# Performance work log

Hardware: AMD Instinct MI355X
Metric: run time of the kernel (lower is better)

Reference implementation:

```python
import jax, jax.numpy as jnp
import numpy as np

N_NODES = 65536
IN_DIM = 256
HIDDEN = 256
NUM_GRAPHS = 128   # B = batch.max()+1; fixed by construction in setup_inputs
MAX_LEN = 1024     # >= max per-graph length (avg 512, binomial tail << 1024)


def _uniform(key, shape, scale):
    return jax.random.uniform(key, shape, jnp.float32, -scale, scale)


def setup_inputs() -> dict:
    key = jax.random.key(0)
    ks = jax.random.split(key, 12)
    x = jax.random.normal(ks[0], (N_NODES, IN_DIM), jnp.float32)
    batch = jnp.sort(jax.random.randint(ks[1], (N_NODES,), 0, NUM_GRAPHS)).astype(jnp.int64)
    s = 1.0 / np.sqrt(HIDDEN)  # torch nn.GRU init: U(-1/sqrt(H), 1/sqrt(H))
    # gate order follows torch: (r, z, n) stacked along first axis -> 3H rows
    params = {
        'W_ih0': _uniform(ks[2], (3 * HIDDEN, IN_DIM), s),
        'W_hh0': _uniform(ks[3], (3 * HIDDEN, HIDDEN), s),
        'b_ih0': _uniform(ks[4], (3 * HIDDEN,), s),
        'b_hh0': _uniform(ks[5], (3 * HIDDEN,), s),
        'W_ih1': _uniform(ks[6], (3 * HIDDEN, HIDDEN), s),
        'W_hh1': _uniform(ks[7], (3 * HIDDEN, HIDDEN), s),
        'b_ih1': _uniform(ks[8], (3 * HIDDEN,), s),
        'b_hh1': _uniform(ks[9], (3 * HIDDEN,), s),
    }
    return {'x': x, 'batch': batch, **params}


def _gru_layer(xs, W_ih, W_hh, b_ih, b_hh):
    # xs: [B, L, D] -> [B, L, H]; torch GRU cell math, gate order (r, z, n)
    B = xs.shape[0]
    H = W_hh.shape[1]
    gx = jnp.einsum('bld,gd->blg', xs, W_ih) + b_ih  # precompute input gates, one big GEMM

    def step(h, gx_t):
        gh = h @ W_hh.T + b_hh
        xr, xz, xn = jnp.split(gx_t, 3, axis=-1)
        hr, hz, hn = jnp.split(gh, 3, axis=-1)
        r = jax.nn.sigmoid(xr + hr)
        z = jax.nn.sigmoid(xz + hz)
        n = jnp.tanh(xn + r * hn)
        h_new = (1.0 - z) * n + z * h
        return h_new, h_new

    h0 = jnp.zeros((B, H), xs.dtype)
    _, hs = jax.lax.scan(step, h0, jnp.swapaxes(gx, 0, 1))  # [L, B, H]
    return jnp.swapaxes(hs, 0, 1)


def reference(x, batch, W_ih0, W_hh0, b_ih0, b_hh0, W_ih1, W_hh1, b_ih1, b_hh1):
    # Ragged per-graph sequences -> padded [B, MAX_LEN, D]. Padding is at the
    # end of each row; GRU is causal so valid positions match the per-graph
    # loop in the original module exactly, and the masked mean ignores padding.
    N, D = x.shape
    b32 = batch.astype(jnp.int32)
    counts = jax.ops.segment_sum(jnp.ones((N,), jnp.float32), b32, num_segments=NUM_GRAPHS)
    starts = jnp.cumsum(counts) - counts              # exclusive prefix sum
    pos = jnp.arange(N, dtype=jnp.float32) - starts[b32]
    pos = pos.astype(jnp.int32)                       # position within graph

    xp = jnp.zeros((NUM_GRAPHS, MAX_LEN, D), x.dtype).at[b32, pos].set(x)
    mask = jnp.zeros((NUM_GRAPHS, MAX_LEN), x.dtype).at[b32, pos].set(1.0)

    h = _gru_layer(xp, W_ih0, W_hh0, b_ih0, b_hh0)
    h = _gru_layer(h, W_ih1, W_hh1, b_ih1, b_hh1)

    denom = jnp.maximum(counts, 1.0)[:, None]
    out = jnp.sum(h * mask[:, :, None], axis=1) / denom  # mean over valid steps
    return out  # dropout is identity at eval
```

## Files before the change

### kernel.cpp

```cpp
#include <hip/hip_runtime.h>
#include <hip/hip_bf16.h>

typedef _Float16 half2_t __attribute__((ext_vector_type(2)));
typedef _Float16 f16x8   __attribute__((ext_vector_type(8)));
typedef float    f32x4   __attribute__((ext_vector_type(4)));
typedef unsigned short u16;
typedef unsigned int   u32;

#define N_NODES 65536
#define IN_DIM  256
#define HIDDEN  256
#define G3      768
#define NGRAPH  128

__device__ __forceinline__ float sigf(float x)    { return 1.f / (1.f + __expf(-x)); }
__device__ __forceinline__ float tanhfast(float x){ return 2.f / (1.f + __expf(-2.f * x)) - 1.f; }

__global__ void k_starts(const int* __restrict__ batch, int* __restrict__ starts, int n, int ngraph) {
    int g = blockIdx.x * blockDim.x + threadIdx.x;
    if (g > ngraph) return;
    int stride = (batch[n - 1] == 0) ? 2 : 1;
    if (g == ngraph) { starts[g] = n; return; }
    int lo = 0, hi = n;
    while (lo < hi) { int mid = (lo + hi) >> 1; if (batch[(size_t)mid * stride] < g) lo = mid + 1; else hi = mid; }
    starts[g] = lo;
}

__global__ void k_cvt8(const float* __restrict__ s, u16* __restrict__ d, int n) {
    int t = blockIdx.x * 256 + threadIdx.x;
    int i = t * 8;
    if (i >= n) return;
    float4 a = ((const float4*)(s + i))[0];
    float4 b = ((const float4*)(s + i))[1];
    f16x8 o;
    o[0] = (_Float16)a.x; o[1] = (_Float16)a.y; o[2] = (_Float16)a.z; o[3] = (_Float16)a.w;
    o[4] = (_Float16)b.x; o[5] = (_Float16)b.y; o[6] = (_Float16)b.z; o[7] = (_Float16)b.w;
    *(f16x8*)(d + i) = o;
}

__global__ void k_bias(const float* __restrict__ bih, const float* __restrict__ bhh, float* __restrict__ o) {
    int i = blockIdx.x * 256 + threadIdx.x;
    if (i < G3) o[i] = bih[i] + (i < 512 ? bhh[i] : 0.f);
}

__global__ void k_swz(const float* __restrict__ W, uint4* __restrict__ out) {
    int t = blockIdx.x * 256 + threadIdx.x;
    if (t >= 24576) return;
    int l = t & 63, kt = (t >> 6) & 7, rest = t >> 9;
    int wv = rest / 6, t6 = rest % 6;
    int row = wv * 96 + t6 * 16 + (l & 15);
    int col = kt * 32 + (l >> 4) * 8;
    const float* s = W + row * 256 + col;
    f16x8 o;
#pragma unroll
    for (int q = 0; q < 8; q++) o[q] = (_Float16)s[q];
    out[t] = __builtin_bit_cast(uint4, o);
}

template <typename AT>
__global__ __launch_bounds__(256) void k_gemm(
    const AT* __restrict__ A, const u16* __restrict__ Bm,
    const float* __restrict__ bias, u16* __restrict__ C,
    int M, int N, int K)
{
    __shared__ u16 As[128 * 40];
    __shared__ u16 Bs[128 * 40];
    const int m0 = blockIdx.y * 128, n0 = blockIdx.x * 128;
    const int t = threadIdx.x;
    const int wave = t >> 6, lane = t & 63;
    const int wm = wave & 1, wn = wave >> 1;
    const int lr = lane & 15, lq = lane >> 4;
    f32x4 acc[4][4] = {};
    const int sr = t >> 1, sp = t & 1;
    const AT*  gA = A  + (size_t)(m0 + sr) * K + sp * 16;
    const u16* gB = Bm + (size_t)(n0 + sr) * K + sp * 16;
    u16* sA = As + sr * 40 + sp * 16;
    u16* sB = Bs + sr * 40 + sp * 16;
    for (int kt = 0; kt < K; kt += 32) {
        uint4 av0, av1;
        if constexpr (sizeof(AT) == 4) {
            float4 a0 = ((const float4*)gA)[0], a1 = ((const float4*)gA)[1];
            float4 a2 = ((const float4*)gA)[2], a3 = ((const float4*)gA)[3];
            f16x8 lo, hi;
            lo[0]=(_Float16)a0.x; lo[1]=(_Float16)a0.y; lo[2]=(_Float16)a0.z; lo[3]=(_Float16)a0.w;
            lo[4]=(_Float16)a1.x; lo[5]=(_Float16)a1.y; lo[6]=(_Float16)a1.z; lo[7]=(_Float16)a1.w;
            hi[0]=(_Float16)a2.x; hi[1]=(_Float16)a2.y; hi[2]=(_Float16)a2.z; hi[3]=(_Float16)a2.w;
            hi[4]=(_Float16)a3.x; hi[5]=(_Float16)a3.y; hi[6]=(_Float16)a3.z; hi[7]=(_Float16)a3.w;
            av0 = __builtin_bit_cast(uint4, lo);
            av1 = __builtin_bit_cast(uint4, hi);
        } else {
            av0 = ((const uint4*)gA)[0];
            av1 = ((const uint4*)gA)[1];
        }
        uint4 b0 = ((const uint4*)gB)[0], b1 = ((const uint4*)gB)[1];
        gA += 32; gB += 32;
        __syncthreads();
        ((uint4*)sA)[0] = av0; ((uint4*)sA)[1] = av1;
        ((uint4*)sB)[0] = b0;  ((uint4*)sB)[1] = b1;
        __syncthreads();
        f16x8 af[4], bf[4];
#pragma unroll
        for (int i = 0; i < 4; i++)
            af[i] = *(const f16x8*)(As + (wm * 64 + i * 16 + lr) * 40 + lq * 8);
#pragma unroll
        for (int j = 0; j < 4; j++)
            bf[j] = *(const f16x8*)(Bs + (wn * 64 + j * 16 + lr) * 40 + lq * 8);
#pragma unroll
        for (int i = 0; i < 4; i++)
#pragma unroll
            for (int j = 0; j < 4; j++)
                acc[i][j] = __builtin_amdgcn_mfma_f32_16x16x32_f16(af[i], bf[j], acc[i][j], 0, 0, 0);
    }
#pragma unroll
    for (int i = 0; i < 4; i++) {
        int row = m0 + wm * 64 + i * 16 + lq * 4;
#pragma unroll
        for (int j = 0; j < 4; j++) {
            int col = n0 + wn * 64 + j * 16 + lr;
            float bv = bias[col];
#pragma unroll
            for (int rr = 0; rr < 4; rr++) {
                _Float16 v = (_Float16)(acc[i][j][rr] + bv);
                C[(size_t)(row + rr) * N + col] = __builtin_bit_cast(u16, v);
            }
        }
    }
}

__global__ __launch_bounds__(512) __attribute__((amdgpu_waves_per_eu(2, 2)))
void k_rec(
    const u16* __restrict__ gx,
    const uint4* __restrict__ wsw,
    const float* __restrict__ bhh,
    const int*   __restrict__ starts,
    u16* __restrict__ hout,
    float* __restrict__ out)
{
    __shared__ float gates[G3];
    __shared__ uint4 hpk4[HIDDEN / 8];
    const int g = blockIdx.x;
    const int tid = threadIdx.x;
    const int l = tid & 63, wv = tid >> 6;
    const int start = starts[g];
    const int len = starts[g + 1] - start;
    if (tid < HIDDEN / 8) hpk4[tid] = make_uint4(0, 0, 0, 0);
    f16x8 wA[6][8];
    {
        const uint4* p = wsw + (size_t)wv * 48 * 64 + l;
#pragma unroll
        for (int t6 = 0; t6 < 6; t6++)
#pragma unroll
            for (int kt = 0; kt < 8; kt++) {
                f16x8 v = __builtin_bit_cast(f16x8, p[(t6 * 8 + kt) * 64]);
                asm volatile("" : "+a"(v));
                wA[t6][kt] = v;
            }
    }
    const _Float16* gxr = (const _Float16*)gx + (size_t)start * G3 + (tid & 255);
    u16* hb = hout ? (hout + (size_t)start * HIDDEN + (tid & 255)) : (u16*)nullptr;
    float hp = 0.f, hs = 0.f;
    const float bn = (tid < 256) ? bhh[512 + tid] : 0.f;
    __syncthreads();
    for (int t = 0; t < len; ++t) {
        float gr = 0.f, gz = 0.f, gn = 0.f;
        if (tid < 256) {
            const _Float16* p = gxr + (size_t)t * G3;
            gr = (float)p[0]; gz = (float)p[256]; gn = (float)p[512];
        }
        f32x4 acc[6];
#pragma unroll
        for (int t6 = 0; t6 < 6; t6++) acc[t6] = (f32x4){0.f, 0.f, 0.f, 0.f};
#pragma unroll
        for (int kt = 0; kt < 8; kt++) {
            f16x8 b = __builtin_bit_cast(f16x8, hpk4[kt * 4 + (l >> 4)]);
#pragma unroll
            for (int t6 = 0; t6 < 6; t6++)
                acc[t6] = __builtin_amdgcn_mfma_f32_16x16x32_f16(wA[t6][kt], b, acc[t6], 0, 0, 0);
        }
        if ((l & 15) == 0) {
            int ro = wv * 96 + (l >> 4) * 4;
#pragma unroll
            for (int t6 = 0; t6 < 6; t6++)
                *(f32x4*)&gates[ro + t6 * 16] = acc[t6];
        }
        __syncthreads();
        if (tid < 256) {
            int h = tid;
            float r = sigf(gr + gates[h]);
            float z = sigf(gz + gates[256 + h]);
            float n = tanhfast(gn + r * (gates[512 + h] + bn));
            float hnew = (1.f - z) * n + z * hp;
            hp = hnew; hs += hnew;
            _Float16 ph = (_Float16)hnew;
            u16 pk = __builtin_bit_cast(u16, ph);
            ((u16*)hpk4)[h] = pk;
            if (hb) hb[(u32)t * HIDDEN] = pk;
        }
        __syncthreads();
    }
    if (out && tid < 256) {
        float inv = 1.f / (float)(len > 0 ? len : 1);
        out[g * HIDDEN + tid] = hs * inv;
    }
}

extern "C" void kernel_launch(void* const* d_in, const int* in_sizes, int n_in,
                              void* d_out, int out_size, void* d_ws, size_t ws_size,
                              hipStream_t stream)
{
    const float* x     = (const float*)d_in[0];
    const int*   batch = (const int*)d_in[1];
    const float* Wih0  = (const float*)d_in[2];
    const float* Whh0  = (const float*)d_in[3];
    const float* bih0  = (const float*)d_in[4];
    const float* bhh0  = (const float*)d_in[5];
    const float* Wih1  = (const float*)d_in[6];
    const float* Whh1  = (const float*)d_in[7];
    const float* bih1  = (const float*)d_in[8];
    const float* bhh1  = (const float*)d_in[9];
    float* out = (float*)d_out;

    char* ws = (char*)d_ws;
    size_t o = 0;
    int*   starts = (int*)  (ws + o); o += 4096;
    float* bias0  = (float*)(ws + o); o += 4096;
    float* bias1  = (float*)(ws + o); o += 4096;
    u16*   wi0    = (u16*)  (ws + o); o += (size_t)G3 * IN_DIM * 2;
    u16*   wi1    = (u16*)  (ws + o); o += (size_t)G3 * HIDDEN * 2;
    uint4* wsw0   = (uint4*)(ws + o); o += (size_t)G3 * HIDDEN * 2;
    uint4* wsw1   = (uint4*)(ws + o); o += (size_t)G3 * HIDDEN * 2;
    u16*   h0     = (u16*)  (ws + o); o += (size_t)N_NODES * HIDDEN * 2;
    u16*   gxbuf  = (u16*)  (ws + o); o += (size_t)N_NODES * G3 * 2;

    k_starts<<<1, 256, 0, stream>>>(batch, starts, N_NODES, NGRAPH);
    k_bias<<<3, 256, 0, stream>>>(bih0, bhh0, bias0);
    k_bias<<<3, 256, 0, stream>>>(bih1, bhh1, bias1);
    k_cvt8<<<96, 256, 0, stream>>>(Wih0, wi0, G3 * IN_DIM);
    k_cvt8<<<96, 256, 0, stream>>>(Wih1, wi1, G3 * HIDDEN);
    k_swz<<<96, 256, 0, stream>>>(Whh0, wsw0);
    k_swz<<<96, 256, 0, stream>>>(Whh1, wsw1);

    k_gemm<float><<<dim3(G3 / 128, N_NODES / 128), 256, 0, stream>>>(x, wi0, bias0, gxbuf, N_NODES, G3, IN_DIM);
    k_rec<<<NGRAPH, 512, 0, stream>>>(gxbuf, wsw0, bhh0, starts, h0, (float*)nullptr);
    k_gemm<_Float16><<<dim3(G3 / 128, N_NODES / 128), 256, 0, stream>>>((const _Float16*)h0, wi1, bias1, gxbuf, N_NODES, G3, HIDDEN);
    k_rec<<<NGRAPH, 512, 0, stream>>>(gxbuf, wsw1, bhh1, starts, (u16*)nullptr, out);
}
```

Baseline: 1.718 ms.

## Halve recurrence block to 4 waves holding W_hh split across AGPRs and VGPRs

```diff
diff --git a/kernel.cpp b/kernel.cpp
--- a/kernel.cpp
+++ b/kernel.cpp
@@ -15,6 +15,13 @@
 
 __device__ __forceinline__ float sigf(float x)    { return 1.f / (1.f + __expf(-x)); }
 __device__ __forceinline__ float tanhfast(float x){ return 2.f / (1.f + __expf(-2.f * x)) - 1.f; }
+
+__device__ __forceinline__ void mfma_a(f32x4& acc, const f16x8& a, const f16x8& b) {
+    asm("v_mfma_f32_16x16x32_f16 %0, %1, %2, %0" : "+v"(acc) : "a"(a), "v"(b));
+}
+__device__ __forceinline__ void mfma_v(f32x4& acc, const f16x8& a, const f16x8& b) {
+    asm("v_mfma_f32_16x16x32_f16 %0, %1, %2, %0" : "+v"(acc) : "v"(a), "v"(b));
+}
 
 __global__ void k_starts(const int* __restrict__ batch, int* __restrict__ starts, int n, int ngraph) {
     int g = blockIdx.x * blockDim.x + threadIdx.x;
@@ -46,9 +53,9 @@
 __global__ void k_swz(const float* __restrict__ W, uint4* __restrict__ out) {
     int t = blockIdx.x * 256 + threadIdx.x;
     if (t >= 24576) return;
-    int l = t & 63, kt = (t >> 6) & 7, rest = t >> 9;
-    int wv = rest / 6, t6 = rest % 6;
-    int row = wv * 96 + t6 * 16 + (l & 15);
+    int l = t & 63, c = t >> 6;
+    int kt = c & 7, t6 = (c >> 3) % 12, wv = c / 96;
+    int row = wv * 192 + t6 * 16 + (l & 15);
     int col = kt * 32 + (l >> 4) * 8;
     const float* s = W + row * 256 + col;
     f16x8 o;
@@ -127,7 +134,7 @@
     }
 }
 
-__global__ __launch_bounds__(512) __attribute__((amdgpu_waves_per_eu(2, 2)))
+__global__ __attribute__((amdgpu_flat_work_group_size(256, 256), amdgpu_waves_per_eu(1, 1)))
 void k_rec(
     const u16* __restrict__ gx,
     const uint4* __restrict__ wsw,
@@ -144,61 +151,74 @@
     const int start = starts[g];
     const int len = starts[g + 1] - start;
     if (tid < HIDDEN / 8) hpk4[tid] = make_uint4(0, 0, 0, 0);
-    f16x8 wA[6][8];
+    f16x8 wa[60], wb[36];
     {
-        const uint4* p = wsw + (size_t)wv * 48 * 64 + l;
-#pragma unroll
-        for (int t6 = 0; t6 < 6; t6++)
-#pragma unroll
-            for (int kt = 0; kt < 8; kt++) {
-                f16x8 v = __builtin_bit_cast(f16x8, p[(t6 * 8 + kt) * 64]);
-                asm volatile("" : "+a"(v));
-                wA[t6][kt] = v;
-            }
-    }
-    const _Float16* gxr = (const _Float16*)gx + (size_t)start * G3 + (tid & 255);
-    u16* hb = hout ? (hout + (size_t)start * HIDDEN + (tid & 255)) : (u16*)nullptr;
+        const uint4* p = wsw + (size_t)wv * 96 * 64 + l;
+#pragma unroll
+        for (int f = 0; f < 60; f++) {
+            f16x8 v = __builtin_bit_cast(f16x8, p[f * 64]);
+            asm volatile("" : "+a"(v));
+            wa[f] = v;
+        }
+#pragma unroll
+        for (int f = 0; f < 36; f++) {
+            f16x8 v = __builtin_bit_cast(f16x8, p[(60 + f) * 64]);
+            asm volatile("" : "+v"(v));
+            wb[f] = v;
+        }
+    }
+    const _Float16* gxr = (const _Float16*)gx + (size_t)start * G3 + tid;
+    u16* hb = hout ? (hout + (size_t)start * HIDDEN + tid) : (u16*)nullptr;
     float hp = 0.f, hs = 0.f;
-    const float bn = (tid < 256) ? bhh[512 + tid] : 0.f;
+    const float bn = bhh[512 + tid];
+    float gr = 0.f, gz = 0.f, gn = 0.f;
+    if (len > 0) { gr = (float)gxr[0]; gz = (float)gxr[256]; gn = (float)gxr[512]; }
+    f32x4 acc[12];
+#pragma unroll
+    for (int t6 = 0; t6 < 12; t6++) acc[t6] = (f32x4){0.f, 0.f, 0.f, 0.f};
     __syncthreads();
     for (int t = 0; t < len; ++t) {
-        float gr = 0.f, gz = 0.f, gn = 0.f;
-        if (tid < 256) {
-            const _Float16* p = gxr + (size_t)t * G3;
-            gr = (float)p[0]; gz = (float)p[256]; gn = (float)p[512];
-        }
-        f32x4 acc[6];
-#pragma unroll
-        for (int t6 = 0; t6 < 6; t6++) acc[t6] = (f32x4){0.f, 0.f, 0.f, 0.f};
+        int tn = t + 1 < len ? t + 1 : len - 1;
+        const _Float16* pp = gxr + (u32)tn * G3;
+        float pr = (float)pp[0], pz = (float)pp[256], pn = (float)pp[512];
 #pragma unroll
         for (int kt = 0; kt < 8; kt++) {
             f16x8 b = __builtin_bit_cast(f16x8, hpk4[kt * 4 + (l >> 4)]);
 #pragma unroll
-            for (int t6 = 0; t6 < 6; t6++)
-                acc[t6] = __builtin_amdgcn_mfma_f32_16x16x32_f16(wA[t6][kt], b, acc[t6], 0, 0, 0);
-        }
+            for (int t6 = 0; t6 < 12; t6++) {
+                const int f = t6 * 8 + kt;
+                if (f < 60) mfma_a(acc[t6], wa[f], b);
+                else        mfma_v(acc[t6], wb[f - 60], b);
+            }
+        }
+        asm volatile("s_nop 7\n\ts_nop 7"
+                     : "+v"(acc[0]), "+v"(acc[1]), "+v"(acc[2]), "+v"(acc[3]),
+                       "+v"(acc[4]), "+v"(acc[5]), "+v"(acc[6]), "+v"(acc[7]),
+                       "+v"(acc[8]), "+v"(acc[9]), "+v"(acc[10]), "+v"(acc[11]));
         if ((l & 15) == 0) {
-            int ro = wv * 96 + (l >> 4) * 4;
-#pragma unroll
-            for (int t6 = 0; t6 < 6; t6++)
+            int ro = wv * 192 + (l >> 4) * 4;
+#pragma unroll
+            for (int t6 = 0; t6 < 12; t6++)
                 *(f32x4*)&gates[ro + t6 * 16] = acc[t6];
         }
-        __syncthreads();
-        if (tid < 256) {
-            int h = tid;
-            float r = sigf(gr + gates[h]);
-            float z = sigf(gz + gates[256 + h]);
-            float n = tanhfast(gn + r * (gates[512 + h] + bn));
+#pragma unroll
+        for (int t6 = 0; t6 < 12; t6++) acc[t6] = (f32x4){0.f, 0.f, 0.f, 0.f};
+        __syncthreads();
+        {
+            float r = sigf(gr + gates[tid]);
+            float z = sigf(gz + gates[256 + tid]);
+            float n = tanhfast(gn + r * (gates[512 + tid] + bn));
             float hnew = (1.f - z) * n + z * hp;
             hp = hnew; hs += hnew;
             _Float16 ph = (_Float16)hnew;
             u16 pk = __builtin_bit_cast(u16, ph);
-            ((u16*)hpk4)[h] = pk;
+            ((u16*)hpk4)[tid] = pk;
             if (hb) hb[(u32)t * HIDDEN] = pk;
-        }
-        __syncthreads();
-    }
-    if (out && tid < 256) {
+            gr = pr; gz = pz; gn = pn;
+        }
+        __syncthreads();
+    }
+    if (out) {
         float inv = 1.f / (float)(len > 0 ? len : 1);
         out[g * HIDDEN + tid] = hs * inv;
     }
@@ -241,7 +261,7 @@
     k_swz<<<96, 256, 0, stream>>>(Whh1, wsw1);
 
     k_gemm<float><<<dim3(G3 / 128, N_NODES / 128), 256, 0, stream>>>(x, wi0, bias0, gxbuf, N_NODES, G3, IN_DIM);
-    k_rec<<<NGRAPH, 512, 0, stream>>>(gxbuf, wsw0, bhh0, starts, h0, (float*)nullptr);
+    k_rec<<<NGRAPH, 256, 0, stream>>>(gxbuf, wsw0, bhh0, starts, h0, (float*)nullptr);
     k_gemm<_Float16><<<dim3(G3 / 128, N_NODES / 128), 256, 0, stream>>>((const _Float16*)h0, wi1, bias1, gxbuf, N_NODES, G3, HIDDEN);
-    k_rec<<<NGRAPH, 512, 0, stream>>>(gxbuf, wsw1, bhh1, starts, (u16*)nullptr, out);
-}
+    k_rec<<<NGRAPH, 256, 0, stream>>>(gxbuf, wsw1, bhh1, starts, (u16*)nullptr, out);
+}
```

Result: slower. 1.856 ms (+8.0%).
